# Kernel tuning notes

Hardware: AMD Instinct MI355X
Metric: run time of the kernel (lower is better)

## Reference

```python
import jax, jax.numpy as jnp
import numpy as np

N = 100000
E = 1600000
IN_C, HID_C, OUT_C = 256, 128, 64


def setup_inputs() -> dict:
    key = jax.random.key(0)
    ks = jax.random.split(key, 8)
    x = jax.random.normal(ks[0], (N, IN_C), dtype=jnp.float32)
    edge_index = jax.random.randint(ks[1], (2, E), 0, N, dtype=jnp.int64)
    # Glorot-ish scale for weights
    W1 = jax.random.normal(ks[2], (IN_C, HID_C), dtype=jnp.float32) * (1.0 / np.sqrt(IN_C))
    b1 = jnp.zeros((HID_C,), dtype=jnp.float32)
    W2 = jax.random.normal(ks[3], (HID_C, OUT_C), dtype=jnp.float32) * (1.0 / np.sqrt(HID_C))
    b2 = jnp.zeros((OUT_C,), dtype=jnp.float32)
    W3 = jax.random.normal(ks[4], (HID_C, OUT_C), dtype=jnp.float32) * (1.0 / np.sqrt(HID_C))
    b3 = jnp.zeros((OUT_C,), dtype=jnp.float32)
    return {"x": x, "edge_index": edge_index, "W1": W1, "b1": b1,
            "W2": W2, "b2": b2, "W3": W3, "b3": b3}


def _gcn_conv(x, W, b, src, dst, num_nodes):
    # GCNConv(normalize=False): linear transform, then scatter-add of
    # source-node messages onto destination nodes, then bias.
    h = x @ W                                   # [N, C_out]
    agg = jax.ops.segment_sum(h[src], dst, num_segments=num_nodes)  # [N, C_out]
    return agg + b


def reference(x, edge_index, W1, b1, W2, b2, W3, b3):
    src = edge_index[0]
    dst = edge_index[1]
    h = jax.nn.relu(_gcn_conv(x, W1, b1, src, dst, N))
    mu = _gcn_conv(h, W2, b2, src, dst, N)
    logvar = _gcn_conv(h, W3, b3, src, dst, N)
    return (mu, logvar)
```

## Files before the change

### kernel.cpp

```cpp
#include <hip/hip_runtime.h>
#include <hip/hip_bf16.h>
#include <cstdint>


#define INC  256
#define HIDC 128
#define OUTC 64

__device__ __forceinline__ int load_idx(const void* p, long long i, int is64) {
  if (is64) return (int)((const long long*)p)[i];
  return ((const int*)p)[i];
}

__global__ void detect_kernel(const unsigned int* __restrict__ p, int* __restrict__ flag) {
  __shared__ int nz;
  if (threadIdx.x == 0) nz = 0;
  __syncthreads();
  unsigned int w = p[2 * threadIdx.x + 1];
  if (w) atomicAdd(&nz, 1);
  __syncthreads();
  if (threadIdx.x == 0) *flag = (nz == 0) ? 1 : 0;
}

__global__ void zero_int_kernel(int* __restrict__ p, int n) {
  int i = blockIdx.x * blockDim.x + threadIdx.x;
  if (i < n) p[i] = 0;
}

__global__ void count_kernel(const void* __restrict__ eidx, int E,
                             const int* __restrict__ flag, int* __restrict__ counts) {
  int is64 = *flag;
  int stride = gridDim.x * blockDim.x;
  for (int e = blockIdx.x * blockDim.x + threadIdx.x; e < E; e += stride) {
    int d = load_idx(eidx, (long long)E + e, is64);
    atomicAdd(&counts[d], 1);
  }
}

__global__ __launch_bounds__(256) void block_sum_kernel(
    const int* __restrict__ counts, int* __restrict__ block_sums, int N) {
  int b = blockIdx.x, t = threadIdx.x;
  int i = b * 256 + t;
  int v = (i < N) ? counts[i] : 0;
#pragma unroll
  for (int off = 32; off >= 1; off >>= 1) v += __shfl_down(v, off, 64);
  __shared__ int ws_[4];
  if ((t & 63) == 0) ws_[t >> 6] = v;
  __syncthreads();
  if (t == 0) block_sums[b] = ws_[0] + ws_[1] + ws_[2] + ws_[3];
}

__global__ __launch_bounds__(512) void scan_blocksums_kernel(
    const int* __restrict__ block_sums, int* __restrict__ block_base, int SB) {
  __shared__ int buf[512];
  int t = threadIdx.x;
  int self = (t < SB) ? block_sums[t] : 0;
  buf[t] = self;
  __syncthreads();
#pragma unroll
  for (int off = 1; off < 512; off <<= 1) {
    int x = (t >= off) ? buf[t - off] : 0;
    __syncthreads();
    buf[t] += x;
    __syncthreads();
  }
  if (t < SB) block_base[t] = buf[t] - self;
}

__global__ __launch_bounds__(256) void scan_local_kernel(
    const int* __restrict__ counts, const int* __restrict__ block_base,
    int* __restrict__ offsets, int N) {
  __shared__ int buf[256];
  int b = blockIdx.x, t = threadIdx.x;
  int i = b * 256 + t;
  int self = (i < N) ? counts[i] : 0;
  buf[t] = self;
  __syncthreads();
#pragma unroll
  for (int off = 1; off < 256; off <<= 1) {
    int x = (t >= off) ? buf[t - off] : 0;
    __syncthreads();
    buf[t] += x;
    __syncthreads();
  }
  int incl = buf[t] + block_base[b];
  if (i < N) offsets[i] = incl - self;
  if (i == N - 1) offsets[N] = incl;
}

__global__ void fill_kernel(const void* __restrict__ eidx, int E,
                            const int* __restrict__ flag, const int* __restrict__ offsets,
                            int* __restrict__ cursor, int* __restrict__ csr_src) {
  int is64 = *flag;
  int stride = gridDim.x * blockDim.x;
  for (int e = blockIdx.x * blockDim.x + threadIdx.x; e < E; e += stride) {
    int s = load_idx(eidx, e, is64);
    int d = load_idx(eidx, (long long)E + e, is64);
    int p = atomicAdd(&cursor[d], 1);
    csr_src[offsets[d] + p] = s;
  }
}

template <int K, bool SPLIT>
__global__ __launch_bounds__(256, 2) void gemm_kernel(
    const float* __restrict__ A, const float* __restrict__ B0,
    const float* __restrict__ B1, const float* __restrict__ bias0,
    const float* __restrict__ bias1, float* __restrict__ out, int M, int Nn) {
  __shared__ float AsT[32][68];
  __shared__ float Bs[32][128];
  const int tid = threadIdx.x;
  const int tx = tid & 15;
  const int ty = tid >> 4;
  const int bm = blockIdx.x * 64;

  float acc[4][8];
#pragma unroll
  for (int i = 0; i < 4; i++)
#pragma unroll
    for (int j = 0; j < 8; j++) acc[i][j] = 0.f;

  for (int k0 = 0; k0 < K; k0 += 32) {
#pragma unroll
    for (int f = tid; f < 512; f += 256) {
      int r = f >> 3, c4 = f & 7;
      int row = bm + r;
      float4 v = make_float4(0.f, 0.f, 0.f, 0.f);
      if (row < M) v = *(const float4*)(A + (long long)row * K + k0 + c4 * 4);
      AsT[c4 * 4 + 0][r] = v.x;
      AsT[c4 * 4 + 1][r] = v.y;
      AsT[c4 * 4 + 2][r] = v.z;
      AsT[c4 * 4 + 3][r] = v.w;
    }
#pragma unroll
    for (int f = tid; f < 1024; f += 256) {
      int r = f >> 5, c4 = f & 31;
      int k = k0 + r;
      int c = c4 * 4;
      float4 v;
      if (!SPLIT) {
        v = *(const float4*)(B0 + (long long)k * 128 + c);
      } else {
        const float* Bp = (c < 64) ? (B0 + (long long)k * 64 + c)
                                   : (B1 + (long long)k * 64 + (c - 64));
        v = *(const float4*)Bp;
      }
      *(float4*)&Bs[r][c] = v;
    }
    __syncthreads();
#pragma unroll
    for (int kk = 0; kk < 32; kk++) {
      float4 av = *(const float4*)(&AsT[kk][ty * 4]);
      float4 b0 = *(const float4*)(&Bs[kk][tx * 8]);
      float4 b1 = *(const float4*)(&Bs[kk][tx * 8 + 4]);
      float a[4] = {av.x, av.y, av.z, av.w};
      float b[8] = {b0.x, b0.y, b0.z, b0.w, b1.x, b1.y, b1.z, b1.w};
#pragma unroll
      for (int i = 0; i < 4; i++)
#pragma unroll
        for (int j = 0; j < 8; j++) acc[i][j] = fmaf(a[i], b[j], acc[i][j]);
    }
    __syncthreads();
  }

#pragma unroll
  for (int i = 0; i < 4; i++) {
    int row = bm + ty * 4 + i;
    if (row >= M) continue;
    int c0 = tx * 8;
    if (!SPLIT) {
      float4 v0 = make_float4(acc[i][0], acc[i][1], acc[i][2], acc[i][3]);
      float4 v1 = make_float4(acc[i][4], acc[i][5], acc[i][6], acc[i][7]);
      *(float4*)(out + (long long)row * 128 + c0) = v0;
      *(float4*)(out + (long long)row * 128 + c0 + 4) = v1;
    } else {
      const float* bb = (c0 < 64) ? bias0 : bias1;
      int cb = c0 & 63;
      long long base = (c0 < 64) ? ((long long)row * 64 + c0)
                                 : ((long long)Nn * 64 + (long long)row * 64 + (c0 - 64));
      float4 v0 = make_float4(acc[i][0] + bb[cb + 0], acc[i][1] + bb[cb + 1],
                              acc[i][2] + bb[cb + 2], acc[i][3] + bb[cb + 3]);
      float4 v1 = make_float4(acc[i][4] + bb[cb + 4], acc[i][5] + bb[cb + 5],
                              acc[i][6] + bb[cb + 6], acc[i][7] + bb[cb + 7]);
      *(float4*)(out + base) = v0;
      *(float4*)(out + base + 4) = v1;
    }
  }
}

template <bool RELU>
__global__ __launch_bounds__(256) void seg_kernel(
    const float* __restrict__ feat, const int* __restrict__ offsets,
    const int* __restrict__ csr_src, const float* __restrict__ bias,
    float* __restrict__ out, int Nn) {
  int n = blockIdx.x * 4 + (threadIdx.x >> 6);
  int lane = threadIdx.x & 63;
  if (n >= Nn) return;
  int lo = offsets[n], hi = offsets[n + 1];
  int c = lane << 1;
  float ax = 0.f, ay = 0.f;
  int i = lo;
  for (; i + 4 <= hi; i += 4) {
    int s0 = csr_src[i];
    int s1 = csr_src[i + 1];
    int s2 = csr_src[i + 2];
    int s3 = csr_src[i + 3];
    float2 v0 = *(const float2*)(feat + (size_t)s0 * HIDC + c);
    float2 v1 = *(const float2*)(feat + (size_t)s1 * HIDC + c);
    float2 v2 = *(const float2*)(feat + (size_t)s2 * HIDC + c);
    float2 v3 = *(const float2*)(feat + (size_t)s3 * HIDC + c);
    ax += v0.x + v1.x + v2.x + v3.x;
    ay += v0.y + v1.y + v2.y + v3.y;
  }
  for (; i < hi; i++) {
    int s = csr_src[i];
    float2 v = *(const float2*)(feat + (size_t)s * HIDC + c);
    ax += v.x;
    ay += v.y;
  }
  if (RELU) {
    ax = fmaxf(ax + bias[c], 0.f);
    ay = fmaxf(ay + bias[c + 1], 0.f);
  }
  *(float2*)(out + (size_t)n * HIDC + c) = make_float2(ax, ay);
}

extern "C" void kernel_launch(void* const* d_in, const int* in_sizes, int n_in,
                              void* d_out, int out_size, void* d_ws, size_t ws_size,
                              hipStream_t stream) {
  const float* x  = (const float*)d_in[0];
  const void*  ei = d_in[1];
  const float* W1 = (const float*)d_in[2];
  const float* b1 = (const float*)d_in[3];
  const float* W2 = (const float*)d_in[4];
  const float* b2 = (const float*)d_in[5];
  const float* W3 = (const float*)d_in[6];
  const float* b3 = (const float*)d_in[7];
  float* out = (float*)d_out;

  const int Nn = in_sizes[0] / INC;
  const int E  = in_sizes[1] / 2;

  const int SB = (Nn + 255) / 256;

  float* h0 = (float*)d_ws;
  float* h  = h0 + (size_t)Nn * HIDC;
  float* agg2 = h0;
  int* offsets = (int*)(h + (size_t)Nn * HIDC);
  int* cnt     = offsets + (Nn + 1);
  int* csr     = cnt + Nn;
  int* flag    = csr + E;
  int* bsums   = flag + 1;
  int* bbase   = bsums + SB;

  const int zb = (Nn + 255) / 256;
  const int eb = 2048;

  hipLaunchKernelGGL(detect_kernel, dim3(1), dim3(256), 0, stream,
                     (const unsigned int*)ei, flag);
  hipLaunchKernelGGL(zero_int_kernel, dim3(zb), dim3(256), 0, stream, cnt, Nn);
  hipLaunchKernelGGL(count_kernel, dim3(eb), dim3(256), 0, stream, ei, E, flag, cnt);
  hipLaunchKernelGGL(block_sum_kernel, dim3(SB), dim3(256), 0, stream, cnt, bsums, Nn);
  hipLaunchKernelGGL(scan_blocksums_kernel, dim3(1), dim3(512), 0, stream, bsums, bbase, SB);
  hipLaunchKernelGGL(scan_local_kernel, dim3(SB), dim3(256), 0, stream, cnt, bbase, offsets, Nn);
  hipLaunchKernelGGL(zero_int_kernel, dim3(zb), dim3(256), 0, stream, cnt, Nn);
  hipLaunchKernelGGL(fill_kernel, dim3(eb), dim3(256), 0, stream, ei, E, flag,
                     offsets, cnt, csr);

  const int mg = (Nn + 63) / 64;
  const int sg = (Nn + 3) / 4;
  hipLaunchKernelGGL((gemm_kernel<INC, false>), dim3(mg), dim3(256), 0, stream,
                     x, W1, nullptr, nullptr, nullptr, h0, Nn, Nn);
  hipLaunchKernelGGL((seg_kernel<true>), dim3(sg), dim3(256), 0, stream,
                     h0, offsets, csr, b1, h, Nn);
  hipLaunchKernelGGL((seg_kernel<false>), dim3(sg), dim3(256), 0, stream,
                     h, offsets, csr, nullptr, agg2, Nn);
  hipLaunchKernelGGL((gemm_kernel<HIDC, true>), dim3(mg), dim3(256), 0, stream,
                     agg2, W2, W3, b2, b3, out, Nn, Nn);
}
```

Before: 674.5 us.

## Register-prefetch next GEMM tile and swizzle shared-memory layout to avoid bank conflicts

```diff
diff --git a/kernel.cpp b/kernel.cpp
--- a/kernel.cpp
+++ b/kernel.cpp
@@ -102,57 +102,99 @@
 }
 
 template <int K, bool SPLIT>
-__global__ __launch_bounds__(256, 2) void gemm_kernel(
+__global__ __launch_bounds__(256) void gemm_kernel(
     const float* __restrict__ A, const float* __restrict__ B0,
     const float* __restrict__ B1, const float* __restrict__ bias0,
     const float* __restrict__ bias1, float* __restrict__ out, int M, int Nn) {
-  __shared__ float AsT[32][68];
-  __shared__ float Bs[32][128];
+  __shared__ float As[64][33];
+  __shared__ float Bs[32 * 128];
   const int tid = threadIdx.x;
   const int tx = tid & 15;
   const int ty = tid >> 4;
   const int bm = blockIdx.x * 64;
 
+  const int ar0 = tid >> 3, ac = (tid & 7) * 4;
+  const int br0 = tid >> 5, bq0 = tid & 31;
+
+  const int q0 = 2 * tx, q1 = 2 * tx + 1;
+  const int o0 = (q0 ^ (q0 >> 3)) * 4;
+  const int o1 = (q1 ^ (q1 >> 3)) * 4;
+
   float acc[4][8];
 #pragma unroll
   for (int i = 0; i < 4; i++)
 #pragma unroll
     for (int j = 0; j < 8; j++) acc[i][j] = 0.f;
 
+  float4 aP[2], bP[4];
+
+#pragma unroll
+  for (int s = 0; s < 2; s++) {
+    int row = bm + ar0 + s * 32;
+    aP[s] = (row < M) ? *(const float4*)(A + (long long)row * K + ac)
+                      : make_float4(0.f, 0.f, 0.f, 0.f);
+  }
+#pragma unroll
+  for (int s = 0; s < 4; s++) {
+    int k = br0 + s * 8;
+    int c = bq0 * 4;
+    if (!SPLIT) {
+      bP[s] = *(const float4*)(B0 + (long long)k * 128 + c);
+    } else {
+      const float* Bp = (c < 64) ? (B0 + (long long)k * 64 + c)
+                                 : (B1 + (long long)k * 64 + (c - 64));
+      bP[s] = *(const float4*)Bp;
+    }
+  }
+
   for (int k0 = 0; k0 < K; k0 += 32) {
 #pragma unroll
-    for (int f = tid; f < 512; f += 256) {
-      int r = f >> 3, c4 = f & 7;
-      int row = bm + r;
-      float4 v = make_float4(0.f, 0.f, 0.f, 0.f);
-      if (row < M) v = *(const float4*)(A + (long long)row * K + k0 + c4 * 4);
-      AsT[c4 * 4 + 0][r] = v.x;
-      AsT[c4 * 4 + 1][r] = v.y;
-      AsT[c4 * 4 + 2][r] = v.z;
-      AsT[c4 * 4 + 3][r] = v.w;
-    }
-#pragma unroll
-    for (int f = tid; f < 1024; f += 256) {
-      int r = f >> 5, c4 = f & 31;
-      int k = k0 + r;
-      int c = c4 * 4;
-      float4 v;
-      if (!SPLIT) {
-        v = *(const float4*)(B0 + (long long)k * 128 + c);
-      } else {
-        const float* Bp = (c < 64) ? (B0 + (long long)k * 64 + c)
-                                   : (B1 + (long long)k * 64 + (c - 64));
-        v = *(const float4*)Bp;
+    for (int s = 0; s < 2; s++) {
+      int r = ar0 + s * 32;
+      As[r][ac + 0] = aP[s].x;
+      As[r][ac + 1] = aP[s].y;
+      As[r][ac + 2] = aP[s].z;
+      As[r][ac + 3] = aP[s].w;
+    }
+#pragma unroll
+    for (int s = 0; s < 4; s++) {
+      int r = br0 + s * 8;
+      int qs = bq0 ^ (bq0 >> 3);
+      *(float4*)&Bs[r * 128 + qs * 4] = bP[s];
+    }
+    __syncthreads();
+
+    if (k0 + 32 < K) {
+      int kn = k0 + 32;
+#pragma unroll
+      for (int s = 0; s < 2; s++) {
+        int row = bm + ar0 + s * 32;
+        aP[s] = (row < M) ? *(const float4*)(A + (long long)row * K + kn + ac)
+                          : make_float4(0.f, 0.f, 0.f, 0.f);
       }
-      *(float4*)&Bs[r][c] = v;
-    }
-    __syncthreads();
+#pragma unroll
+      for (int s = 0; s < 4; s++) {
+        int k = kn + br0 + s * 8;
+        int c = bq0 * 4;
+        if (!SPLIT) {
+          bP[s] = *(const float4*)(B0 + (long long)k * 128 + c);
+        } else {
+          const float* Bp = (c < 64) ? (B0 + (long long)k * 64 + c)
+                                     : (B1 + (long long)k * 64 + (c - 64));
+          bP[s] = *(const float4*)Bp;
+        }
+      }
+    }
+
 #pragma unroll
     for (int kk = 0; kk < 32; kk++) {
-      float4 av = *(const float4*)(&AsT[kk][ty * 4]);
-      float4 b0 = *(const float4*)(&Bs[kk][tx * 8]);
-      float4 b1 = *(const float4*)(&Bs[kk][tx * 8 + 4]);
-      float a[4] = {av.x, av.y, av.z, av.w};
+      float a0 = As[ty * 4 + 0][kk];
+      float a1 = As[ty * 4 + 1][kk];
+      float a2 = As[ty * 4 + 2][kk];
+      float a3 = As[ty * 4 + 3][kk];
+      float4 b0 = *(const float4*)&Bs[kk * 128 + o0];
+      float4 b1 = *(const float4*)&Bs[kk * 128 + o1];
+      float a[4] = {a0, a1, a2, a3};
       float b[8] = {b0.x, b0.y, b0.z, b0.w, b1.x, b1.y, b1.z, b1.w};
 #pragma unroll
       for (int i = 0; i < 4; i++)
```

New measurement: 708.7 us. 5.1% more time.
